# Kernel optimization log

Measured on AMD Instinct MI355X. Metric: run time of the kernel, lower is better.

## Reference

```python
import jax, jax.numpy as jnp
import numpy as np
import math

B, C, P = 128, 512, 196   # batch, cnn_channels, spatial positions
T = 32                    # caption length
V = 10403                 # n_tokens
E = 128                   # emb_size
U = 256                   # lstm_units


def setup_inputs() -> dict:
    key = jax.random.key(0)
    ks = jax.random.split(key, 16)
    s = 0.02
    return {
        "image_features": jax.random.normal(ks[0], (B, C, P), jnp.float32),
        "captions_ix": jax.random.randint(ks[1], (B, T), 0, V),
        "W_h0": jax.random.normal(ks[2], (U, C), jnp.float32) * s,
        "b_h0": jnp.zeros((U,), jnp.float32),
        "W_c0": jax.random.normal(ks[3], (U, C), jnp.float32) * s,
        "b_c0": jnp.zeros((U,), jnp.float32),
        "W_key": jax.random.normal(ks[4], (U, C), jnp.float32) * s,
        "b_key": jnp.zeros((U,), jnp.float32),
        "emb": jax.random.normal(ks[5], (V, E), jnp.float32) * s,
        "W_ih": jax.random.normal(ks[6], (4 * U, E + C), jnp.float32) * s,
        "b_ih": jnp.zeros((4 * U,), jnp.float32),
        "W_hh": jax.random.normal(ks[7], (4 * U, U), jnp.float32) * s,
        "b_hh": jnp.zeros((4 * U,), jnp.float32),
        "W_out": jax.random.normal(ks[8], (V, U + C + E), jnp.float32) * s,
        "b_out": jnp.zeros((V,), jnp.float32),
    }


def reference(image_features, captions_ix, W_h0, b_h0, W_c0, b_c0, W_key, b_key,
              emb, W_ih, b_ih, W_hh, b_hh, W_out, b_out):
    mean_feat = image_features.mean(axis=2)           # [B, C]
    c0 = mean_feat @ W_c0.T + b_c0                    # [B, U] initial cell
    h0 = mean_feat @ W_h0.T + b_h0                    # [B, U] initial hidden
    values = image_features.transpose(0, 2, 1)        # [B, P, C]
    keys = values @ W_key.T + b_key                   # [B, P, U]
    cap_emb = emb[captions_ix]                        # [B, T, E]
    emb_seq = cap_emb.transpose(1, 0, 2)              # [T, B, E] for scan
    scale = 1.0 / math.sqrt(U)

    def step(carry, emb_t):
        h, c, q = carry
        # scaled dot-product attention, query = prev hidden (cell at t=0)
        scores = jnp.einsum('bu,bpu->bp', q, keys) * scale       # [B, P]
        w = jax.nn.softmax(scores, axis=-1)                      # [B, P]
        attn = jnp.einsum('bp,bpc->bc', w, values)               # [B, C]
        x = jnp.concatenate([emb_t, attn], axis=1)               # [B, E+C]
        gates = x @ W_ih.T + b_ih + h @ W_hh.T + b_hh            # [B, 4U]
        i_g, f_g, g_g, o_g = jnp.split(gates, 4, axis=1)
        c_new = jax.nn.sigmoid(f_g) * c + jax.nn.sigmoid(i_g) * jnp.tanh(g_g)
        h_new = jax.nn.sigmoid(o_g) * jnp.tanh(c_new)
        logit = jnp.concatenate([attn, emb_t, h_new], axis=1) @ W_out.T + b_out
        return (h_new, c_new, h_new), (logit, w)

    # NB: at t=0 the original queries with initial_cell (not hidden).
    _, (logits, maps) = jax.lax.scan(step, (h0, c0, c0), emb_seq)
    logits = logits.transpose(1, 0, 2)   # [B, T, V]
    maps = maps.transpose(1, 0, 2)       # [B, T, P]
    return logits, maps
```

## Files before the change

kernel.cpp:

```cpp
#include <hip/hip_runtime.h>
#include <stdint.h>

#define B_   128
#define C_   512
#define P_   196
#define PP_  200
#define T_   32
#define V_   10403
#define E_   128
#define U_   256
#define KX_  896
#define K2_  1792
#define NPAD_ 10496
#define WLD_ 904

typedef unsigned short u16;
typedef __attribute__((ext_vector_type(8))) short bf16x8;
typedef __attribute__((ext_vector_type(4))) float f32x4;

__device__ __forceinline__ float b2f(u16 u){
  union { unsigned int i; float f; } v; v.i = ((unsigned int)u) << 16; return v.f;
}
__device__ __forceinline__ u16 f2b(float f){
  union { float f; unsigned int i; } v; v.f = f;
  unsigned int r = (v.i + 0x7FFFu + ((v.i >> 16) & 1u)) >> 16;
  return (u16)r;
}
__device__ __forceinline__ unsigned int dup(float a){
  return (unsigned int)f2b(a) * 0x00010001u;
}
__device__ __forceinline__ unsigned int hl(float w){
  u16 h = f2b(w);
  float lo = w - b2f(h);
  return (unsigned int)h | ((unsigned int)f2b(lo) << 16);
}

__global__ void k_prep(const float* __restrict__ imf, float* __restrict__ mean,
                       u16* __restrict__ imb){
  int idx = blockIdx.x * 256 + threadIdx.x;
  const float4* p4 = (const float4*)(imf + (size_t)idx * P_);
  u16* orow = imb + (size_t)idx * PP_;
  float s = 0.f;
  for (int i = 0; i < 49; ++i){
    float4 q = p4[i];
    s += q.x + q.y + q.z + q.w;
    ushort4 o;
    o.x = f2b(q.x); o.y = f2b(q.y); o.z = f2b(q.z); o.w = f2b(q.w);
    *((ushort4*)(orow + 4 * i)) = o;
  }
  ushort4 z; z.x = z.y = z.z = z.w = 0;
  *((ushort4*)(orow + 196)) = z;
  mean[idx] = s * (1.f / 196.f);
}

__global__ void k_h0c0(const float* __restrict__ mean,
                       const float* __restrict__ Wh, const float* __restrict__ bh,
                       const float* __restrict__ Wc, const float* __restrict__ bc,
                       float* __restrict__ h0, float* __restrict__ c0,
                       unsigned int* __restrict__ h0b){
  int idx = blockIdx.x * 256 + threadIdx.x;
  int b = idx >> 9, j = idx & 511;
  int u = j & 255, isc = j >> 8;
  const float* wr = (isc ? Wc : Wh) + (size_t)u * C_;
  const float* m = mean + b * C_;
  float s = 0.f;
  for (int c = 0; c < C_; ++c) s += m[c] * wr[c];
  s += (isc ? bc : bh)[u];
  (isc ? c0 : h0)[b * U_ + u] = s;
  if (!isc) h0b[b * U_ + u] = dup(s);
}

__global__ void k_wkeyb(const float* __restrict__ Wk, u16* __restrict__ WkB){
  int idx = blockIdx.x * 256 + threadIdx.x;
  WkB[idx] = f2b(Wk[idx]);
}

__global__ void k_wgb(const float* __restrict__ Wih, const float* __restrict__ Whh,
                      u16* __restrict__ Wg){
  int idx = blockIdx.x * 256 + threadIdx.x;
  int j = idx / 896, k = idx - j * 896;
  float w;
  if (k < 512)      w = Wih[(size_t)j * 640 + 128 + k];
  else if (k < 640) w = Wih[(size_t)j * 640 + (k - 512)];
  else              w = Whh[(size_t)j * 256 + (k - 640)];
  Wg[(size_t)j * 896 + k] = f2b(w);
}

__global__ void k_xemb(const int* __restrict__ cap, const float* __restrict__ emb,
                       unsigned int* __restrict__ X){
  int idx = blockIdx.x * 256 + threadIdx.x;
  int row = idx >> 7, e = idx & 127;
  int ix = cap[row];
  X[(size_t)row * KX_ + C_ + e] = dup(emb[(size_t)ix * E_ + e]);
}

__global__ void __launch_bounds__(256) k_keys(
    const float* __restrict__ imf, const u16* __restrict__ WkeyB,
    u16* __restrict__ keysT)
{
  __shared__ __align__(16) u16 Bs[16 * 40];
  int tid = threadIdx.x;
  int p0 = blockIdx.x * 16;
  int b  = blockIdx.y;
  int lane = tid & 63, wv = tid >> 6;
  int quad = lane >> 4, l15 = lane & 15;
  f32x4 acc[4];
  #pragma unroll
  for (int m = 0; m < 4; ++m) acc[m] = (f32x4){0.f, 0.f, 0.f, 0.f};
  for (int kc = 0; kc < 16; ++kc){
    int k0 = kc * 32;
    #pragma unroll
    for (int e = tid; e < 512; e += 256){
      int kk = e >> 4, pp = e & 15;
      int p = p0 + pp;
      float v = (p < P_) ? imf[((size_t)b * C_ + (k0 + kk)) * P_ + p] : 0.f;
      Bs[pp * 40 + kk] = f2b(v);
    }
    __syncthreads();
    bf16x8 bfrag = *((const bf16x8*)(Bs + l15 * 40 + quad * 8));
    #pragma unroll
    for (int m = 0; m < 4; ++m){
      int u = wv * 64 + m * 16 + l15;
      bf16x8 afrag = *((const bf16x8*)(WkeyB + (size_t)u * C_ + k0 + quad * 8));
      acc[m] = __builtin_amdgcn_mfma_f32_16x16x32_bf16(afrag, bfrag, acc[m], 0, 0, 0);
    }
    __syncthreads();
  }
  int p = p0 + l15;
  if (p < P_){
    #pragma unroll
    for (int m = 0; m < 4; ++m){
      ushort4 o;
      o.x = f2b(acc[m][0]); o.y = f2b(acc[m][1]);
      o.z = f2b(acc[m][2]); o.w = f2b(acc[m][3]);
      *((ushort4*)(keysT + ((size_t)b * P_ + p) * U_ + wv * 64 + m * 16 + quad * 4)) = o;
    }
  }
}

__global__ void __launch_bounds__(256) k_attn4(
    const u16* __restrict__ imb, const u16* __restrict__ keysT,
    const float* __restrict__ qsrc, const int* __restrict__ cap,
    const float* __restrict__ emb, unsigned int* __restrict__ X,
    float* __restrict__ maps, int t)
{
  __shared__ __align__(16) float qs[U_];
  __shared__ __align__(16) float red[256];
  __shared__ __align__(16) float wl[256];
  int b = blockIdx.x, half = blockIdx.y, tid = threadIdx.x;
  qs[tid] = qsrc[b * U_ + tid];
  __syncthreads();
  float s = -1e30f;
  if (tid < P_){
    const u16* kp = keysT + ((size_t)b * P_ + tid) * U_;
    float acc = 0.f;
    #pragma unroll
    for (int i = 0; i < 32; ++i){
      bf16x8 v8 = *((const bf16x8*)(kp + i * 8));
      #pragma unroll
      for (int j = 0; j < 8; ++j) acc += qs[i * 8 + j] * b2f((u16)v8[j]);
    }
    s = acc * 0.0625f;
  }
  red[tid] = s; __syncthreads();
  for (int off = 128; off > 0; off >>= 1){
    if (tid < off) red[tid] = fmaxf(red[tid], red[tid + off]);
    __syncthreads();
  }
  float mx = red[0]; __syncthreads();
  float e = (tid < P_) ? __expf(s - mx) : 0.f;
  red[tid] = e; __syncthreads();
  for (int off = 128; off > 0; off >>= 1){
    if (tid < off) red[tid] += red[tid + off];
    __syncthreads();
  }
  float inv = 1.f / red[0];
  float w = e * inv;
  wl[tid] = w;
  if (half == 0 && tid < P_)
    maps[(size_t)(b * T_ + t) * P_ + tid] = w;
  __syncthreads();
  size_t xrow = (size_t)(b * T_ + t) * KX_;
  int c = half * 256 + tid;
  {
    const u16* vrow = imb + ((size_t)b * C_ + c) * PP_;
    float a = 0.f;
    #pragma unroll
    for (int i = 0; i < 25; ++i){
      bf16x8 v8 = *((const bf16x8*)(vrow + i * 8));
      #pragma unroll
      for (int j = 0; j < 8; ++j) a += wl[i * 8 + j] * b2f((u16)v8[j]);
    }
    X[xrow + c] = dup(a);
  }
  if (half == 0 && tid < E_){
    int ix = cap[b * T_ + t];
    X[xrow + C_ + tid] = dup(emb[(size_t)ix * E_ + tid]);
  }
}

__global__ void __launch_bounds__(256) k_gates3(
    const u16* __restrict__ Wg, const float* __restrict__ bih,
    const float* __restrict__ bhh, const unsigned int* __restrict__ h0b,
    float* __restrict__ c_st, float* __restrict__ hnew,
    unsigned int* X, int t)
{
  __shared__ __align__(16) u16 wls[64 * WLD_];
  __shared__ __align__(16) u16 xls[16 * WLD_];
  __shared__ __align__(16) float gl[4 * 16 * 16];
  int tid = threadIdx.x;
  int b0 = (blockIdx.x >> 4) * 16;
  int u0 = (blockIdx.x & 15) * 16;
  for (int e = tid; e < 16 * 224; e += 256){
    int r = e / 224, q4 = e - r * 224;
    const unsigned int* src;
    if (q4 < 160)       src = X + ((size_t)((b0 + r) * T_ + t)) * KX_ + q4 * 4;
    else if (t > 0)     src = X + ((size_t)((b0 + r) * T_ + t - 1)) * KX_ + q4 * 4;
    else                src = h0b + (b0 + r) * U_ + (q4 * 4 - 640);
    uint4 v = *((const uint4*)src);
    ushort4 o;
    o.x = (u16)v.x; o.y = (u16)v.y; o.z = (u16)v.z; o.w = (u16)v.w;
    *((ushort4*)(xls + r * WLD_ + q4 * 4)) = o;
  }
  for (int e = tid; e < 64 * 112; e += 256){
    int jl = e / 112, s8 = e - jl * 112;
    int j = ((jl >> 4) << 8) + u0 + (jl & 15);
    uint4 v = *((const uint4*)(Wg + (size_t)j * 896 + s8 * 8));
    *((uint4*)(wls + jl * WLD_ + s8 * 8)) = v;
  }
  __syncthreads();
  int lane = tid & 63, wv = tid >> 6;
  int quad = lane >> 4, l15 = lane & 15;
  f32x4 acc = {0.f, 0.f, 0.f, 0.f};
  #pragma unroll
  for (int kc = 0; kc < 28; ++kc){
    bf16x8 af  = *((const bf16x8*)(xls + l15 * WLD_ + kc * 32 + quad * 8));
    bf16x8 bfv = *((const bf16x8*)(wls + (wv * 16 + l15) * WLD_ + kc * 32 + quad * 8));
    acc = __builtin_amdgcn_mfma_f32_16x16x32_bf16(af, bfv, acc, 0, 0, 0);
  }
  #pragma unroll
  for (int r = 0; r < 4; ++r)
    gl[(wv << 8) + ((quad * 4 + r) << 4) + l15] = acc[r];
  __syncthreads();
  {
    int br = tid >> 4, ur = tid & 15;
    int b = b0 + br, u = u0 + ur;
    float i_g = gl[(0 << 8) + (br << 4) + ur] + bih[u]       + bhh[u];
    float f_g = gl[(1 << 8) + (br << 4) + ur] + bih[256 + u] + bhh[256 + u];
    float g_g = gl[(2 << 8) + (br << 4) + ur] + bih[512 + u] + bhh[512 + u];
    float o_g = gl[(3 << 8) + (br << 4) + ur] + bih[768 + u] + bhh[768 + u];
    float cold = c_st[b * U_ + u];
    float si = 1.f / (1.f + __expf(-i_g));
    float sf = 1.f / (1.f + __expf(-f_g));
    float so = 1.f / (1.f + __expf(-o_g));
    float cn = sf * cold + si * tanhf(g_g);
    float hn = so * tanhf(cn);
    c_st[b * U_ + u] = cn;
    hnew[b * U_ + u] = hn;
    X[(size_t)(b * T_ + t) * KX_ + 640 + u] = dup(hn);
  }
}

__global__ void k_wsplit(const float* __restrict__ Wout,
                         unsigned int* __restrict__ W2){
  int idx = blockIdx.x * 256 + threadIdx.x;
  int v = idx / 224, kq = idx - v * 224;
  uint4 o;
  if (v < V_){
    float4 w = ((const float4*)(Wout + (size_t)v * KX_))[kq];
    o.x = hl(w.x); o.y = hl(w.y); o.z = hl(w.z); o.w = hl(w.w);
  } else {
    o.x = o.y = o.z = o.w = 0u;
  }
  ((uint4*)(W2 + (size_t)v * KX_))[kq] = o;
}

__global__ void __launch_bounds__(256) k_logits(
    const u16* __restrict__ A2, const u16* __restrict__ W2,
    const float* __restrict__ bout, float* __restrict__ out)
{
  __shared__ __align__(16) u16 As[128 * 32];
  __shared__ __align__(16) u16 Bs[128 * 32];
  int tid = threadIdx.x;
  int n0 = blockIdx.x * 128;
  int m0 = blockIdx.y * 128;
  int lane = tid & 63, wv = tid >> 6;
  int wm = wv >> 1, wn = wv & 1;
  int quad = lane >> 4, l15 = lane & 15;

  f32x4 acc[4][4];
  #pragma unroll
  for (int i = 0; i < 4; ++i)
    #pragma unroll
    for (int j = 0; j < 4; ++j)
      acc[i][j] = (f32x4){0.f, 0.f, 0.f, 0.f};

  int rsub = tid >> 2, seg = tid & 3;
  const u16* ga0 = A2 + (size_t)(m0 + rsub)      * K2_ + seg * 8;
  const u16* ga1 = A2 + (size_t)(m0 + 64 + rsub) * K2_ + seg * 8;
  const u16* gb0 = W2 + (size_t)(n0 + rsub)      * K2_ + seg * 8;
  const u16* gb1 = W2 + (size_t)(n0 + 64 + rsub) * K2_ + seg * 8;
  u16* lA0 = As + tid * 8;
  u16* lA1 = As + (256 + tid) * 8;
  u16* lB0 = Bs + tid * 8;
  u16* lB1 = Bs + (256 + tid) * 8;

  const u16* arow0 = As + (wm * 64 + l15) * 32 + quad * 8;
  const u16* brow0 = Bs + (wn * 64 + l15) * 32 + quad * 8;

  for (int kc = 0; kc < 56; ++kc){
    __builtin_amdgcn_global_load_lds(ga0, lA0, 16, 0, 0);
    __builtin_amdgcn_global_load_lds(ga1, lA1, 16, 0, 0);
    __builtin_amdgcn_global_load_lds(gb0, lB0, 16, 0, 0);
    __builtin_amdgcn_global_load_lds(gb1, lB1, 16, 0, 0);
    ga0 += 32; ga1 += 32; gb0 += 32; gb1 += 32;
    __syncthreads();
    bf16x8 a[4], b[4];
    #pragma unroll
    for (int i = 0; i < 4; ++i)
      a[i] = *((const bf16x8*)(arow0 + i * 16 * 32));
    #pragma unroll
    for (int j = 0; j < 4; ++j)
      b[j] = *((const bf16x8*)(brow0 + j * 16 * 32));
    #pragma unroll
    for (int i = 0; i < 4; ++i)
      #pragma unroll
      for (int j = 0; j < 4; ++j)
        acc[i][j] = __builtin_amdgcn_mfma_f32_16x16x32_bf16(a[i], b[j], acc[i][j], 0, 0, 0);
    __syncthreads();
  }

  int orow = m0 + wm * 64 + quad * 4;
  #pragma unroll
  for (int j = 0; j < 4; ++j){
    int v = n0 + wn * 64 + j * 16 + l15;
    if (v < V_){
      float bo = bout[v];
      #pragma unroll
      for (int i = 0; i < 4; ++i){
        #pragma unroll
        for (int r = 0; r < 4; ++r)
          out[(size_t)(orow + i * 16 + r) * V_ + v] = acc[i][j][r] + bo;
      }
    }
  }
}

extern "C" void kernel_launch(void* const* d_in, const int* in_sizes, int n_in,
                              void* d_out, int out_size, void* d_ws, size_t ws_size,
                              hipStream_t stream)
{
  const float* imf  = (const float*)d_in[0];
  const int*   cap  = (const int*)d_in[1];
  const float* Wh0  = (const float*)d_in[2];
  const float* bh0  = (const float*)d_in[3];
  const float* Wc0  = (const float*)d_in[4];
  const float* bc0  = (const float*)d_in[5];
  const float* Wkey = (const float*)d_in[6];
  const float* emb  = (const float*)d_in[8];
  const float* Wih  = (const float*)d_in[9];
  const float* bih  = (const float*)d_in[10];
  const float* Whh  = (const float*)d_in[11];
  const float* bhh  = (const float*)d_in[12];
  const float* Wout = (const float*)d_in[13];
  const float* bout = (const float*)d_in[14];

  float* mean  = (float*)d_ws;
  float* hbuf0 = mean  + 65536;
  float* hbuf1 = hbuf0 + 32768;
  float* cbuf  = hbuf1 + 32768;
  unsigned int* h0b = (unsigned int*)(cbuf + 32768);
  unsigned int* X   = h0b + 32768;
  unsigned int* W2  = X + (size_t)4096 * KX_;
  u16* Wg    = (u16*)(W2 + (size_t)NPAD_ * KX_);
  u16* WkeyB = Wg + (size_t)1024 * 896;
  u16* keysT = WkeyB + 131072;
  u16* imb   = keysT + (size_t)B_ * P_ * U_;

  float* out  = (float*)d_out;
  float* maps = out + (size_t)B_ * T_ * V_;

  k_wsplit<<<9184, 256, 0, stream>>>(Wout, W2);
  k_wgb<<<3584, 256, 0, stream>>>(Wih, Whh, Wg);
  k_wkeyb<<<512, 256, 0, stream>>>(Wkey, WkeyB);
  k_prep<<<256, 256, 0, stream>>>(imf, mean, imb);
  k_keys<<<dim3(13, 128), 256, 0, stream>>>(imf, WkeyB, keysT);
  k_h0c0<<<256, 256, 0, stream>>>(mean, Wh0, bh0, Wc0, bc0, hbuf0, cbuf, h0b);
  k_xemb<<<2048, 256, 0, stream>>>(cap, emb, X);
  for (int t = 0; t < T_; ++t){
    const float* q  = (t == 0) ? cbuf : ((t & 1) ? hbuf1 : hbuf0);
    float*       hn = (t & 1) ? hbuf0 : hbuf1;
    k_attn4<<<dim3(128, 2), 256, 0, stream>>>(imb, keysT, q, cap, emb,
                                              X, maps, t);
    k_gates3<<<128, 256, 0, stream>>>(Wg, bih, bhh, h0b, cbuf, hn, X, t);
  }
  k_logits<<<dim3(82, 32), 256, 0, stream>>>((const u16*)X, (const u16*)W2,
                                             bout, out);
}
```

Measured before the change: 1.550 ms.

## Fuse recurrent attention and gates steps into one persistent kernel with grid barriers

The 64 per-step launches (attention plus gates for each of 32 time steps) become a single persistent kernel of 128 blocks. Steps are separated by atomic-counter grid barriers, and the counter is reset in the embedding kernel. The gate weight slice is loaded into LDS once instead of every step, which removes repeated weight traffic as well as per-launch overhead. In exchange, attention runs on 128 blocks instead of 256, each block doing both channel halves, and the kernel relies on all blocks being co-resident for the spin barrier to work.

Measured after the change: 2.747 ms. +77.2%, slower.

```diff
diff --git a/kernel.cpp b/kernel.cpp
--- a/kernel.cpp
+++ b/kernel.cpp
@@ -13,6 +13,7 @@
 #define K2_  1792
 #define NPAD_ 10496
 #define WLD_ 904
+#define NBLK_ 128
 
 typedef unsigned short u16;
 typedef __attribute__((ext_vector_type(8))) short bf16x8;
@@ -87,8 +88,9 @@
 }
 
 __global__ void k_xemb(const int* __restrict__ cap, const float* __restrict__ emb,
-                       unsigned int* __restrict__ X){
-  int idx = blockIdx.x * 256 + threadIdx.x;
+                       unsigned int* __restrict__ X, unsigned int* __restrict__ bar){
+  int idx = blockIdx.x * 256 + threadIdx.x;
+  if (idx == 0) *bar = 0u;
   int row = idx >> 7, e = idx & 127;
   int ix = cap[row];
   X[(size_t)row * KX_ + C_ + e] = dup(emb[(size_t)ix * E_ + e]);
@@ -138,126 +140,150 @@
   }
 }
 
-__global__ void __launch_bounds__(256) k_attn4(
+__global__ void __launch_bounds__(256) k_loopf(
     const u16* __restrict__ imb, const u16* __restrict__ keysT,
-    const float* __restrict__ qsrc, const int* __restrict__ cap,
-    const float* __restrict__ emb, unsigned int* __restrict__ X,
-    float* __restrict__ maps, int t)
-{
-  __shared__ __align__(16) float qs[U_];
-  __shared__ __align__(16) float red[256];
-  __shared__ __align__(16) float wl[256];
-  int b = blockIdx.x, half = blockIdx.y, tid = threadIdx.x;
-  qs[tid] = qsrc[b * U_ + tid];
-  __syncthreads();
-  float s = -1e30f;
-  if (tid < P_){
-    const u16* kp = keysT + ((size_t)b * P_ + tid) * U_;
-    float acc = 0.f;
-    #pragma unroll
-    for (int i = 0; i < 32; ++i){
-      bf16x8 v8 = *((const bf16x8*)(kp + i * 8));
-      #pragma unroll
-      for (int j = 0; j < 8; ++j) acc += qs[i * 8 + j] * b2f((u16)v8[j]);
-    }
-    s = acc * 0.0625f;
-  }
-  red[tid] = s; __syncthreads();
-  for (int off = 128; off > 0; off >>= 1){
-    if (tid < off) red[tid] = fmaxf(red[tid], red[tid + off]);
-    __syncthreads();
-  }
-  float mx = red[0]; __syncthreads();
-  float e = (tid < P_) ? __expf(s - mx) : 0.f;
-  red[tid] = e; __syncthreads();
-  for (int off = 128; off > 0; off >>= 1){
-    if (tid < off) red[tid] += red[tid + off];
-    __syncthreads();
-  }
-  float inv = 1.f / red[0];
-  float w = e * inv;
-  wl[tid] = w;
-  if (half == 0 && tid < P_)
-    maps[(size_t)(b * T_ + t) * P_ + tid] = w;
-  __syncthreads();
-  size_t xrow = (size_t)(b * T_ + t) * KX_;
-  int c = half * 256 + tid;
-  {
-    const u16* vrow = imb + ((size_t)b * C_ + c) * PP_;
-    float a = 0.f;
-    #pragma unroll
-    for (int i = 0; i < 25; ++i){
-      bf16x8 v8 = *((const bf16x8*)(vrow + i * 8));
-      #pragma unroll
-      for (int j = 0; j < 8; ++j) a += wl[i * 8 + j] * b2f((u16)v8[j]);
-    }
-    X[xrow + c] = dup(a);
-  }
-  if (half == 0 && tid < E_){
-    int ix = cap[b * T_ + t];
-    X[xrow + C_ + tid] = dup(emb[(size_t)ix * E_ + tid]);
-  }
-}
-
-__global__ void __launch_bounds__(256) k_gates3(
     const u16* __restrict__ Wg, const float* __restrict__ bih,
     const float* __restrict__ bhh, const unsigned int* __restrict__ h0b,
-    float* __restrict__ c_st, float* __restrict__ hnew,
-    unsigned int* X, int t)
+    float* __restrict__ c_st, float* __restrict__ hbuf0,
+    float* __restrict__ hbuf1, unsigned int* X, float* __restrict__ maps,
+    unsigned int* bar)
 {
   __shared__ __align__(16) u16 wls[64 * WLD_];
   __shared__ __align__(16) u16 xls[16 * WLD_];
   __shared__ __align__(16) float gl[4 * 16 * 16];
-  int tid = threadIdx.x;
-  int b0 = (blockIdx.x >> 4) * 16;
-  int u0 = (blockIdx.x & 15) * 16;
-  for (int e = tid; e < 16 * 224; e += 256){
-    int r = e / 224, q4 = e - r * 224;
-    const unsigned int* src;
-    if (q4 < 160)       src = X + ((size_t)((b0 + r) * T_ + t)) * KX_ + q4 * 4;
-    else if (t > 0)     src = X + ((size_t)((b0 + r) * T_ + t - 1)) * KX_ + q4 * 4;
-    else                src = h0b + (b0 + r) * U_ + (q4 * 4 - 640);
-    uint4 v = *((const uint4*)src);
-    ushort4 o;
-    o.x = (u16)v.x; o.y = (u16)v.y; o.z = (u16)v.z; o.w = (u16)v.w;
-    *((ushort4*)(xls + r * WLD_ + q4 * 4)) = o;
-  }
+  __shared__ __align__(16) float qs[256];
+  __shared__ __align__(16) float red[256];
+  __shared__ __align__(16) float wl[256];
+  int blk = blockIdx.x, tid = threadIdx.x;
+  int b0 = (blk >> 4) * 16;
+  int u0 = (blk & 15) * 16;
+  int lane = tid & 63, wv = tid >> 6;
+  int quad = lane >> 4, l15 = lane & 15;
+
   for (int e = tid; e < 64 * 112; e += 256){
     int jl = e / 112, s8 = e - jl * 112;
     int j = ((jl >> 4) << 8) + u0 + (jl & 15);
     uint4 v = *((const uint4*)(Wg + (size_t)j * 896 + s8 * 8));
     *((uint4*)(wls + jl * WLD_ + s8 * 8)) = v;
   }
-  __syncthreads();
-  int lane = tid & 63, wv = tid >> 6;
-  int quad = lane >> 4, l15 = lane & 15;
-  f32x4 acc = {0.f, 0.f, 0.f, 0.f};
-  #pragma unroll
-  for (int kc = 0; kc < 28; ++kc){
-    bf16x8 af  = *((const bf16x8*)(xls + l15 * WLD_ + kc * 32 + quad * 8));
-    bf16x8 bfv = *((const bf16x8*)(wls + (wv * 16 + l15) * WLD_ + kc * 32 + quad * 8));
-    acc = __builtin_amdgcn_mfma_f32_16x16x32_bf16(af, bfv, acc, 0, 0, 0);
-  }
-  #pragma unroll
-  for (int r = 0; r < 4; ++r)
-    gl[(wv << 8) + ((quad * 4 + r) << 4) + l15] = acc[r];
-  __syncthreads();
-  {
-    int br = tid >> 4, ur = tid & 15;
-    int b = b0 + br, u = u0 + ur;
-    float i_g = gl[(0 << 8) + (br << 4) + ur] + bih[u]       + bhh[u];
-    float f_g = gl[(1 << 8) + (br << 4) + ur] + bih[256 + u] + bhh[256 + u];
-    float g_g = gl[(2 << 8) + (br << 4) + ur] + bih[512 + u] + bhh[512 + u];
-    float o_g = gl[(3 << 8) + (br << 4) + ur] + bih[768 + u] + bhh[768 + u];
-    float cold = c_st[b * U_ + u];
-    float si = 1.f / (1.f + __expf(-i_g));
-    float sf = 1.f / (1.f + __expf(-f_g));
-    float so = 1.f / (1.f + __expf(-o_g));
-    float cn = sf * cold + si * tanhf(g_g);
-    float hn = so * tanhf(cn);
-    c_st[b * U_ + u] = cn;
-    hnew[b * U_ + u] = hn;
-    X[(size_t)(b * T_ + t) * KX_ + 640 + u] = dup(hn);
+
+  unsigned int btgt = 0;
+  for (int t = 0; t < T_; ++t){
+    const float* qsrc = (t == 0) ? c_st : ((t & 1) ? hbuf1 : hbuf0);
+    float*       hn   = (t & 1) ? hbuf0 : hbuf1;
+
+    {
+      int b = blk;
+      qs[tid] = qsrc[b * U_ + tid];
+      __syncthreads();
+      float s = -1e30f;
+      if (tid < P_){
+        const u16* kp = keysT + ((size_t)b * P_ + tid) * U_;
+        float acc = 0.f;
+        #pragma unroll
+        for (int i = 0; i < 32; ++i){
+          bf16x8 v8 = *((const bf16x8*)(kp + i * 8));
+          #pragma unroll
+          for (int j = 0; j < 8; ++j) acc += qs[i * 8 + j] * b2f((u16)v8[j]);
+        }
+        s = acc * 0.0625f;
+      }
+      red[tid] = s; __syncthreads();
+      for (int off = 128; off > 0; off >>= 1){
+        if (tid < off) red[tid] = fmaxf(red[tid], red[tid + off]);
+        __syncthreads();
+      }
+      float mx = red[0]; __syncthreads();
+      float e = (tid < P_) ? __expf(s - mx) : 0.f;
+      red[tid] = e; __syncthreads();
+      for (int off = 128; off > 0; off >>= 1){
+        if (tid < off) red[tid] += red[tid + off];
+        __syncthreads();
+      }
+      float inv = 1.f / red[0];
+      float w = e * inv;
+      wl[tid] = w;
+      if (tid < P_)
+        maps[(size_t)(b * T_ + t) * P_ + tid] = w;
+      __syncthreads();
+      size_t xrow = (size_t)(b * T_ + t) * KX_;
+      #pragma unroll
+      for (int cc = 0; cc < 2; ++cc){
+        int c = cc * 256 + tid;
+        const u16* vrow = imb + ((size_t)b * C_ + c) * PP_;
+        float a = 0.f;
+        #pragma unroll
+        for (int i = 0; i < 25; ++i){
+          bf16x8 v8 = *((const bf16x8*)(vrow + i * 8));
+          #pragma unroll
+          for (int j = 0; j < 8; ++j) a += wl[i * 8 + j] * b2f((u16)v8[j]);
+        }
+        X[xrow + c] = dup(a);
+      }
+    }
+    __threadfence();
+    __syncthreads();
+    btgt += NBLK_;
+    if (tid == 0){
+      __hip_atomic_fetch_add(bar, 1u, __ATOMIC_ACQ_REL, __HIP_MEMORY_SCOPE_AGENT);
+      while (__hip_atomic_load(bar, __ATOMIC_ACQUIRE, __HIP_MEMORY_SCOPE_AGENT) < btgt)
+        __builtin_amdgcn_s_sleep(2);
+    }
+    __syncthreads();
+    __threadfence();
+
+    {
+      for (int e = tid; e < 16 * 224; e += 256){
+        int r = e / 224, q4 = e - r * 224;
+        const unsigned int* src;
+        if (q4 < 160)       src = X + ((size_t)((b0 + r) * T_ + t)) * KX_ + q4 * 4;
+        else if (t > 0)     src = X + ((size_t)((b0 + r) * T_ + t - 1)) * KX_ + q4 * 4;
+        else                src = h0b + (b0 + r) * U_ + (q4 * 4 - 640);
+        uint4 v = *((const uint4*)src);
+        ushort4 o;
+        o.x = (u16)v.x; o.y = (u16)v.y; o.z = (u16)v.z; o.w = (u16)v.w;
+        *((ushort4*)(xls + r * WLD_ + q4 * 4)) = o;
+      }
+      __syncthreads();
+      f32x4 acc = {0.f, 0.f, 0.f, 0.f};
+      #pragma unroll
+      for (int kc = 0; kc < 28; ++kc){
+        bf16x8 af  = *((const bf16x8*)(xls + l15 * WLD_ + kc * 32 + quad * 8));
+        bf16x8 bfv = *((const bf16x8*)(wls + (wv * 16 + l15) * WLD_ + kc * 32 + quad * 8));
+        acc = __builtin_amdgcn_mfma_f32_16x16x32_bf16(af, bfv, acc, 0, 0, 0);
+      }
+      #pragma unroll
+      for (int r = 0; r < 4; ++r)
+        gl[(wv << 8) + ((quad * 4 + r) << 4) + l15] = acc[r];
+      __syncthreads();
+      {
+        int br = tid >> 4, ur = tid & 15;
+        int b = b0 + br, u = u0 + ur;
+        float i_g = gl[(0 << 8) + (br << 4) + ur] + bih[u]       + bhh[u];
+        float f_g = gl[(1 << 8) + (br << 4) + ur] + bih[256 + u] + bhh[256 + u];
+        float g_g = gl[(2 << 8) + (br << 4) + ur] + bih[512 + u] + bhh[512 + u];
+        float o_g = gl[(3 << 8) + (br << 4) + ur] + bih[768 + u] + bhh[768 + u];
+        float cold = c_st[b * U_ + u];
+        float si = 1.f / (1.f + __expf(-i_g));
+        float sf = 1.f / (1.f + __expf(-f_g));
+        float so = 1.f / (1.f + __expf(-o_g));
+        float cn = sf * cold + si * tanhf(g_g);
+        float hnv = so * tanhf(cn);
+        c_st[b * U_ + u] = cn;
+        hn[b * U_ + u] = hnv;
+        X[(size_t)(b * T_ + t) * KX_ + 640 + u] = dup(hnv);
+      }
+    }
+    __threadfence();
+    __syncthreads();
+    btgt += NBLK_;
+    if (tid == 0){
+      __hip_atomic_fetch_add(bar, 1u, __ATOMIC_ACQ_REL, __HIP_MEMORY_SCOPE_AGENT);
+      while (__hip_atomic_load(bar, __ATOMIC_ACQUIRE, __HIP_MEMORY_SCOPE_AGENT) < btgt)
+        __builtin_amdgcn_s_sleep(2);
+    }
+    __syncthreads();
+    __threadfence();
   }
 }
 
@@ -370,7 +396,8 @@
   float* hbuf1 = hbuf0 + 32768;
   float* cbuf  = hbuf1 + 32768;
   unsigned int* h0b = (unsigned int*)(cbuf + 32768);
-  unsigned int* X   = h0b + 32768;
+  unsigned int* bar = h0b + 32768;
+  unsigned int* X   = bar + 256;
   unsigned int* W2  = X + (size_t)4096 * KX_;
   u16* Wg    = (u16*)(W2 + (size_t)NPAD_ * KX_);
   u16* WkeyB = Wg + (size_t)1024 * 896;
@@ -386,14 +413,11 @@
   k_prep<<<256, 256, 0, stream>>>(imf, mean, imb);
   k_keys<<<dim3(13, 128), 256, 0, stream>>>(imf, WkeyB, keysT);
   k_h0c0<<<256, 256, 0, stream>>>(mean, Wh0, bh0, Wc0, bc0, hbuf0, cbuf, h0b);
-  k_xemb<<<2048, 256, 0, stream>>>(cap, emb, X);
-  for (int t = 0; t < T_; ++t){
-    const float* q  = (t == 0) ? cbuf : ((t & 1) ? hbuf1 : hbuf0);
-    float*       hn = (t & 1) ? hbuf0 : hbuf1;
-    k_attn4<<<dim3(128, 2), 256, 0, stream>>>(imb, keysT, q, cap, emb,
-                                              X, maps, t);
-    k_gates3<<<128, 256, 0, stream>>>(Wg, bih, bhh, h0b, cbuf, hn, X, t);
-  }
+  k_xemb<<<2048, 256, 0, stream>>>(cap, emb, X, bar);
+
+  k_loopf<<<NBLK_, 256, 0, stream>>>((const u16*)imb, keysT, Wg, bih, bhh,
+                                     h0b, cbuf, hbuf0, hbuf1, X, maps, bar);
+
   k_logits<<<dim3(82, 32), 256, 0, stream>>>((const u16*)X, (const u16*)W2,
                                              bout, out);
 }
```
